# Kernel optimization log

Hardware: AMD Instinct MI355X
Metric: run time of the kernel (lower is better)

Reference implementation:

```python
import jax, jax.numpy as jnp
import numpy as np
import math

def setup_inputs() -> dict:
    key = jax.random.key(0)
    k1, k2, k3 = jax.random.split(key, 3)
    B, S, E = 2, 2048, 1024
    H, D = 16, 64
    inputs = jax.random.normal(k1, (B, S, E), dtype=jnp.float32)
    Wqkv = jax.random.uniform(k2, (E, 3 * H * D), minval=-0.1, maxval=0.1, dtype=jnp.float32)
    Wo = jax.random.uniform(k3, (H * D, E), minval=-0.1, maxval=0.1, dtype=jnp.float32)
    return {"inputs": inputs, "Wqkv": Wqkv, "Wo": Wo, "nhead": H}

def reference(inputs, Wqkv, Wo, nhead):
    B, S, E = inputs.shape
    H = int(nhead)
    D = Wqkv.shape[1] // (3 * H)
    causal, ghost = True, True

    qkv = jnp.matmul(inputs, Wqkv)                       # (B, S, 3*H*D)
    qkv = qkv.reshape(B, S, 3, H, D)
    Q = qkv[:, :, 0].transpose(0, 2, 1, 3)               # (B, H, S, D)
    K = qkv[:, :, 1].transpose(0, 2, 1, 3)
    V = qkv[:, :, 2].transpose(0, 2, 1, 3)

    scores = jnp.einsum('bhqd,bhkd->bhqk', Q, K) / math.sqrt(D)
    if causal:
        neg_inf = jnp.float32(-jnp.inf)
        mask = jnp.where(jnp.triu(jnp.ones((S, S), dtype=bool), k=1), neg_inf, jnp.float32(0.0))
        scores = scores + mask  # broadcast over (B, H)

    # ghost softmax: standard stable softmax but denominator gets +1
    z = jnp.exp(scores - jnp.max(scores, axis=-1, keepdims=True))
    denom = jnp.sum(z, axis=-1, keepdims=True)
    if ghost:
        denom = denom + jnp.float32(1.0)
    attn = z / denom                                      # (B, H, S, S)

    A = jnp.einsum('bhqk,bhkd->bhqd', attn, V)            # (B, H, S, D)
    A = A.transpose(0, 2, 1, 3).reshape(B, S, H * D)      # (B, S, H*D)
    return jnp.matmul(A, Wo)
```

## Files before the change

### kernel.cpp

```cpp
#include <hip/hip_runtime.h>

typedef float    f32x4  __attribute__((ext_vector_type(4)));
typedef _Float16 half8  __attribute__((ext_vector_type(8)));
typedef _Float16 half4v __attribute__((ext_vector_type(4)));

#define MFMA16(a,b,c) __builtin_amdgcn_mfma_f32_16x16x32_f16(a,b,c,0,0,0)

__device__ __forceinline__ float exp2_fast(float x){
  float y; asm("v_exp_f32 %0, %1" : "=v"(y) : "v"(x)); return y;
}
__device__ __forceinline__ void gload_lds16(const _Float16* g, _Float16* l){
  __builtin_amdgcn_global_load_lds(
      (const __attribute__((address_space(1))) unsigned int*)(g),
      (__attribute__((address_space(3))) unsigned int*)(l),
      16, 0, 0);
}

#define S_LEN 2048
#define E_DIM 1024
#define H_NUM 16
#define D_DIM 64
#define NBH   32
#define M_ROWS 4096
#define N3    3072
#define LOG2E 1.44269504089f

__global__ void cast_x_kernel(const float* __restrict__ in,
                              _Float16* __restrict__ hi, int n4){
  int i = blockIdx.x * 256 + threadIdx.x;
  if (i >= n4) return;
  const float4 v = reinterpret_cast<const float4*>(in)[i];
  half4v h;
  h[0] = (_Float16)v.x; h[1] = (_Float16)v.y;
  h[2] = (_Float16)v.z; h[3] = (_Float16)v.w;
  *reinterpret_cast<half4v*>(&hi[i*4]) = h;
}

__global__ void transpose_half(const float* __restrict__ in,
                               _Float16* __restrict__ hi, int R, int C){
  __shared__ float tile[32][33];
  int bx = blockIdx.x * 32, by = blockIdx.y * 32;
  int tx = threadIdx.x & 31, ty = threadIdx.x >> 5;
#pragma unroll
  for (int i = ty; i < 32; i += 8)
    tile[i][tx] = in[(size_t)(by + i) * C + bx + tx];
  __syncthreads();
#pragma unroll
  for (int i = ty; i < 32; i += 8)
    hi[(size_t)(bx + i) * R + by + tx] = (_Float16)tile[tx][i];
}

template<int EPI>
__global__ __launch_bounds__(256, 3) void gemm97(
    const _Float16* __restrict__ A, const _Float16* __restrict__ B,
    int Kdim, int Ndim, float* __restrict__ Cout,
    _Float16* __restrict__ qh, _Float16* __restrict__ kh, _Float16* __restrict__ vh)
{
  __shared__ __align__(16) _Float16 sA[128][64], sB[128][64];
  const int tid = threadIdx.x;
  const int m0 = blockIdx.y * 128, n0 = blockIdx.x * 128;
  const int wid = tid >> 6, lane = tid & 63;
  const int wr = (wid >> 1) * 64, wc = (wid & 1) * 64;
  const int lr = lane & 15, lc = lane >> 4;
  const int ldrow = lane >> 3;
  const int ldcol = ((lane & 7) ^ ldrow) * 8;
  const int swz = (lr & 7) << 4;

  f32x4 acc[4][4] = {};
  const int nK = Kdim >> 6;
  for (int ks = 0; ks < nK; ++ks){
    const int k0 = ks << 6;
#pragma unroll
    for (int cc = 0; cc < 4; ++cc){
      const int c = wid * 4 + cc;
      const int row = c * 8 + ldrow;
      gload_lds16(&A[(size_t)(m0 + row) * Kdim + k0 + ldcol], &sA[c*8][0]);
      gload_lds16(&B[(size_t)(n0 + row) * Kdim + k0 + ldcol], &sB[c*8][0]);
    }
    __syncthreads();
    const char* ab = (const char*)&sA[0][0];
    const char* bb = (const char*)&sB[0][0];
#pragma unroll
    for (int kk = 0; kk < 64; kk += 32){
      half8 fa[4], fb[4];
#pragma unroll
      for (int t = 0; t < 4; ++t){
        fa[t] = *reinterpret_cast<const half8*>(
            ab + (wr + t*16 + lr)*128 + ((kk*2 + lc*16) ^ swz));
        fb[t] = *reinterpret_cast<const half8*>(
            bb + (wc + t*16 + lr)*128 + ((kk*2 + lc*16) ^ swz));
      }
#pragma unroll
      for (int mt = 0; mt < 4; ++mt)
#pragma unroll
        for (int nt = 0; nt < 4; ++nt)
          acc[mt][nt] = MFMA16(fa[mt], fb[nt], acc[mt][nt]);
    }
    __syncthreads();
  }
#pragma unroll
  for (int mt = 0; mt < 4; ++mt)
#pragma unroll
    for (int nt = 0; nt < 4; ++nt)
#pragma unroll
      for (int r = 0; r < 4; ++r){
        const int m = m0 + wr + mt*16 + lc*4 + r;
        const int n = n0 + wc + nt*16 + lr;
        float v = acc[mt][nt][r];
        if (EPI == 0){
          Cout[(size_t)m * Ndim + n] = v;
        } else {
          const int t = n >> 10, rem = n & 1023, hh = rem >> 6, d = rem & 63;
          const int b = m >> 11, s = m & 2047;
          const int bh = b * H_NUM + hh;
          if (t == 0) v *= (0.125f * LOG2E);
          size_t o;
          if (t == 2)  o = ((size_t)bh * D_DIM + d) * S_LEN + s;
          else         o = ((size_t)bh * S_LEN + s) * D_DIM + d;
          _Float16* ph = (t == 0) ? qh : (t == 1) ? kh : vh;
          ph[o] = (_Float16)v;
        }
      }
}

__global__ __launch_bounds__(256, 4) void attn_kernel(
    const _Float16* __restrict__ Qh, const _Float16* __restrict__ Kh,
    const _Float16* __restrict__ Vth, _Float16* __restrict__ Ao)
{
  __shared__ __align__(16) _Float16 sK[2][64][64], sV[2][64][64];
  __shared__ __align__(16) _Float16 sP[4][16][64];
  const int tid = threadIdx.x, wid = tid >> 6, lane = tid & 63;
  const int id  = blockIdx.x + 32 * blockIdx.y;
  const int xcd = id & 7, seq = id >> 3;
  const int bh  = xcd + 8 * (seq & 3);
  const int g = seq >> 2, hsel = g & 7, bsel = g >> 3;
  const int qt = (bsel == 0) ? 31 - hsel
               : (bsel == 1) ? hsel
               : (bsel == 2) ? 23 - hsel
                             : 8 + hsel;
  const int q0 = qt * 64;
  const int nT = qt + 1;
  const int lr = lane & 15, lc = lane >> 4;
  const int swz = (lr & 7) << 4;
  const size_t base = (size_t)bh * S_LEN * D_DIM;

  const int lrow = lane >> 3;
  const int cswz = ((lane & 7) ^ lrow) * 8;

  auto stage = [&](int t, int b){
    const int kv0 = t * 64;
#pragma unroll
    for (int cc = 0; cc < 2; ++cc){
      const int c = wid * 2 + cc;
      const int row = c * 8 + lrow;
      gload_lds16(&Kh[base + (size_t)(kv0 + row) * D_DIM + cswz], &sK[b][c*8][0]);
      gload_lds16(&Vth[base + (size_t)row * S_LEN + kv0 + cswz], &sV[b][c*8][0]);
    }
  };

  const int b = bh >> 4, hh = bh & 15;

  half8 fq[2];
  {
    const int qrow = q0 + wid*16 + lr;
#pragma unroll
    for (int kc = 0; kc < 2; ++kc)
      fq[kc] = *reinterpret_cast<const half8*>(&Qh[base + (size_t)qrow * 64 + kc*32 + lc*8]);
  }

  f32x4 acc[4] = {};
  float m = -1e30f, l = 0.f, tm = -1e30f;

  stage(0, 0);
  __syncthreads();

  int cur = 0;
  for (int t = 0; t < nT; ++t){
    if (t + 1 < nT) stage(t + 1, cur ^ 1);

    const char* kb = (const char*)&sK[cur][0][0];
    f32x4 sc[4];
    __builtin_amdgcn_s_setprio(1);
#pragma unroll
    for (int nt = 0; nt < 4; ++nt){
      f32x4 z = {};
#pragma unroll
      for (int kc = 0; kc < 2; ++kc){
        const half8 fk = *reinterpret_cast<const half8*>(
            kb + (nt*16 + lr)*128 + ((kc*64 + lc*16) ^ swz));
        z = MFMA16(fk, fq[kc], z);
      }
      sc[nt] = z;
    }
    __builtin_amdgcn_s_setprio(0);

    if (t == qt){
#pragma unroll
      for (int nt = 0; nt < 4; ++nt)
#pragma unroll
        for (int r = 0; r < 4; ++r)
          if (nt*16 + lc*4 + r > wid*16 + lr) sc[nt][r] = -1e30f;
    }

    f32x4 a;
#pragma unroll
    for (int j = 0; j < 4; ++j)
      a[j] = fmaxf(fmaxf(sc[0][j], sc[1][j]), fmaxf(sc[2][j], sc[3][j]));
    float mx = fmaxf(fmaxf(a[0], a[1]), fmaxf(a[2], a[3]));
    mx = fmaxf(mx, __shfl_xor(mx, 16));
    mx = fmaxf(mx, __shfl_xor(mx, 32));
    tm = fmaxf(tm, mx);

    if (__any(mx > m + 8.0f)){
      const float mn = fmaxf(m, mx);
      const float s = exp2_fast(m - mn);
      l *= s; m = mn;
      float rs[4];
#pragma unroll
      for (int r = 0; r < 4; ++r)
        rs[r] = __shfl(s, (lc << 4) | (lc*4 + r), 64);
#pragma unroll
      for (int dt = 0; dt < 4; ++dt)
#pragma unroll
        for (int r = 0; r < 4; ++r) acc[dt][r] *= rs[r];
    }

    f32x4 ssum = {};
#pragma unroll
    for (int nt = 0; nt < 4; ++nt){
#pragma unroll
      for (int r = 0; r < 4; ++r) sc[nt][r] = exp2_fast(sc[nt][r] - m);
      ssum += sc[nt];
    }
    float s1 = (ssum[0] + ssum[1]) + (ssum[2] + ssum[3]);
    s1 += __shfl_xor(s1, 16);
    s1 += __shfl_xor(s1, 32);
    l += s1;

    char* pw = (char*)&sP[wid][0][0];
#pragma unroll
    for (int nt = 0; nt < 4; ++nt){
      int2 pk;
      pk.x = __builtin_bit_cast(int, __builtin_amdgcn_cvt_pkrtz(sc[nt][0], sc[nt][1]));
      pk.y = __builtin_bit_cast(int, __builtin_amdgcn_cvt_pkrtz(sc[nt][2], sc[nt][3]));
      *reinterpret_cast<int2*>(pw + lr*128 + ((nt*32 + lc*8) ^ swz)) = pk;
    }

    const half8 pa0 = *reinterpret_cast<const half8*>(pw + lr*128 + ((lc*16) ^ swz));
    const half8 pa1 = *reinterpret_cast<const half8*>(pw + lr*128 + ((64 + lc*16) ^ swz));
    const char* vb = (const char*)&sV[cur][0][0];
    __builtin_amdgcn_s_setprio(1);
#pragma unroll
    for (int dt = 0; dt < 4; ++dt){
#pragma unroll
      for (int kc = 0; kc < 2; ++kc){
        const half8 fv = *reinterpret_cast<const half8*>(
            vb + (dt*16 + lr)*128 + ((kc*64 + lc*16) ^ swz));
        acc[dt] = MFMA16(kc ? pa1 : pa0, fv, acc[dt]);
      }
    }
    __builtin_amdgcn_s_setprio(0);

    __syncthreads();
    cur ^= 1;
  }

  const float den = l + exp2_fast(tm - m);
  float rden[4];
#pragma unroll
  for (int r = 0; r < 4; ++r)
    rden[r] = __shfl(den, (lc << 4) | (lc*4 + r), 64);
#pragma unroll
  for (int dt = 0; dt < 4; ++dt)
#pragma unroll
    for (int r = 0; r < 4; ++r){
      const float o = acc[dt][r] / rden[r];
      const int q = q0 + wid*16 + lc*4 + r;
      const int d = dt*16 + lr;
      Ao[((size_t)(b*S_LEN + q)) * E_DIM + hh*D_DIM + d] = (_Float16)o;
    }
}

extern "C" void kernel_launch(void* const* d_in, const int* in_sizes, int n_in,
                              void* d_out, int out_size, void* d_ws, size_t ws_size,
                              hipStream_t stream){
  const float* X    = (const float*)d_in[0];
  const float* Wqkv = (const float*)d_in[1];
  const float* Wo   = (const float*)d_in[2];
  float* out = (float*)d_out;

  _Float16* w = (_Float16*)d_ws;
  size_t off = 0;
  auto alloc = [&](size_t n){ _Float16* p = w + off; off += n; return p; };
  const size_t ME   = (size_t)M_ROWS * E_DIM;
  const size_t WQ   = (size_t)N3 * E_DIM;
  const size_t WOsz = (size_t)E_DIM * E_DIM;
  const size_t QK   = (size_t)NBH * S_LEN * D_DIM;
  _Float16 *Xh = alloc(ME);
  _Float16 *Wqh = alloc(WQ);
  _Float16 *Woh = alloc(WOsz);
  _Float16 *Qh = alloc(QK), *Kh = alloc(QK), *Vth = alloc(QK);
  _Float16 *Ahalf = alloc(ME);

  cast_x_kernel<<<(int)(ME/4/256), 256, 0, stream>>>(X, Xh, (int)(ME/4));
  transpose_half<<<dim3(N3/32, E_DIM/32), 256, 0, stream>>>(Wqkv, Wqh, E_DIM, N3);
  transpose_half<<<dim3(E_DIM/32, E_DIM/32), 256, 0, stream>>>(Wo, Woh, E_DIM, E_DIM);

  gemm97<1><<<dim3(N3/128, M_ROWS/128), 256, 0, stream>>>(
      Xh, Wqh, E_DIM, N3, nullptr, Qh, Kh, Vth);

  attn_kernel<<<dim3(32, NBH), 256, 0, stream>>>(Qh, Kh, Vth, Ahalf);

  gemm97<0><<<dim3(E_DIM/128, M_ROWS/128), 256, 0, stream>>>(
      Ahalf, Woh, E_DIM, E_DIM, out, nullptr, nullptr, nullptr);
}
```

Before: 124.3 us.

## Single-buffer V in attention and use 64-row tiles for output projection GEMM

Attention now double-buffers only K and keeps a single V buffer. V for the current tile is loaded at the start of each iteration and waited on with an explicit vmcnt plus barrier before the PV MFMAs, which cuts LDS use per block and may allow more resident blocks. The output projection switches to a new 64x128-tile GEMM kernel, doubling the grid from 256 to 512 blocks to fill more CUs. The risks are that V load latency is only partly hidden behind the QK and softmax work, and the new GEMM has no double buffering.

```diff
diff --git a/kernel.cpp b/kernel.cpp
--- a/kernel.cpp
+++ b/kernel.cpp
@@ -123,11 +123,76 @@
       }
 }
 
+__global__ __launch_bounds__(256, 4) void gemm64(
+    const _Float16* __restrict__ A, const _Float16* __restrict__ B,
+    int Kdim, int Ndim, float* __restrict__ Cout)
+{
+  __shared__ __align__(16) _Float16 sA[64][64], sB[128][64];
+  const int tid = threadIdx.x;
+  const int m0 = blockIdx.y * 64, n0 = blockIdx.x * 128;
+  const int wid = tid >> 6, lane = tid & 63;
+  const int wr = (wid >> 1) * 32, wc = (wid & 1) * 64;
+  const int lr = lane & 15, lc = lane >> 4;
+  const int ldrow = lane >> 3;
+  const int ldcol = ((lane & 7) ^ ldrow) * 8;
+  const int swz = (lr & 7) << 4;
+
+  f32x4 acc[2][4] = {};
+  const int nK = Kdim >> 6;
+  for (int ks = 0; ks < nK; ++ks){
+    const int k0 = ks << 6;
+#pragma unroll
+    for (int cc = 0; cc < 2; ++cc){
+      const int c = wid * 2 + cc;
+      const int row = c * 8 + ldrow;
+      gload_lds16(&A[(size_t)(m0 + row) * Kdim + k0 + ldcol], &sA[c*8][0]);
+    }
+#pragma unroll
+    for (int cc = 0; cc < 4; ++cc){
+      const int c = wid * 4 + cc;
+      const int row = c * 8 + ldrow;
+      gload_lds16(&B[(size_t)(n0 + row) * Kdim + k0 + ldcol], &sB[c*8][0]);
+    }
+    __syncthreads();
+    const char* ab = (const char*)&sA[0][0];
+    const char* bb = (const char*)&sB[0][0];
+#pragma unroll
+    for (int kk = 0; kk < 64; kk += 32){
+      half8 fa[2], fb[4];
+#pragma unroll
+      for (int t = 0; t < 2; ++t)
+        fa[t] = *reinterpret_cast<const half8*>(
+            ab + (wr + t*16 + lr)*128 + ((kk*2 + lc*16) ^ swz));
+#pragma unroll
+      for (int t = 0; t < 4; ++t)
+        fb[t] = *reinterpret_cast<const half8*>(
+            bb + (wc + t*16 + lr)*128 + ((kk*2 + lc*16) ^ swz));
+#pragma unroll
+      for (int mt = 0; mt < 2; ++mt)
+#pragma unroll
+        for (int nt = 0; nt < 4; ++nt)
+          acc[mt][nt] = MFMA16(fa[mt], fb[nt], acc[mt][nt]);
+    }
+    __syncthreads();
+  }
+#pragma unroll
+  for (int mt = 0; mt < 2; ++mt)
+#pragma unroll
+    for (int nt = 0; nt < 4; ++nt)
+#pragma unroll
+      for (int r = 0; r < 4; ++r){
+        const int m = m0 + wr + mt*16 + lc*4 + r;
+        const int n = n0 + wc + nt*16 + lr;
+        Cout[(size_t)m * Ndim + n] = acc[mt][nt][r];
+      }
+}
+
 __global__ __launch_bounds__(256, 4) void attn_kernel(
     const _Float16* __restrict__ Qh, const _Float16* __restrict__ Kh,
     const _Float16* __restrict__ Vth, _Float16* __restrict__ Ao)
 {
-  __shared__ __align__(16) _Float16 sK[2][64][64], sV[2][64][64];
+  __shared__ __align__(16) _Float16 sK[2][64][64];
+  __shared__ __align__(16) _Float16 sV[64][64];
   __shared__ __align__(16) _Float16 sP[4][16][64];
   const int tid = threadIdx.x, wid = tid >> 6, lane = tid & 63;
   const int id  = blockIdx.x + 32 * blockIdx.y;
@@ -147,14 +212,22 @@
   const int lrow = lane >> 3;
   const int cswz = ((lane & 7) ^ lrow) * 8;
 
-  auto stage = [&](int t, int b){
+  auto stageK = [&](int t, int b){
     const int kv0 = t * 64;
 #pragma unroll
     for (int cc = 0; cc < 2; ++cc){
       const int c = wid * 2 + cc;
       const int row = c * 8 + lrow;
       gload_lds16(&Kh[base + (size_t)(kv0 + row) * D_DIM + cswz], &sK[b][c*8][0]);
-      gload_lds16(&Vth[base + (size_t)row * S_LEN + kv0 + cswz], &sV[b][c*8][0]);
+    }
+  };
+  auto stageV = [&](int t){
+    const int kv0 = t * 64;
+#pragma unroll
+    for (int cc = 0; cc < 2; ++cc){
+      const int c = wid * 2 + cc;
+      const int row = c * 8 + lrow;
+      gload_lds16(&Vth[base + (size_t)row * S_LEN + kv0 + cswz], &sV[c*8][0]);
     }
   };
 
@@ -171,12 +244,13 @@
   f32x4 acc[4] = {};
   float m = -1e30f, l = 0.f, tm = -1e30f;
 
-  stage(0, 0);
+  stageK(0, 0);
   __syncthreads();
 
   int cur = 0;
   for (int t = 0; t < nT; ++t){
-    if (t + 1 < nT) stage(t + 1, cur ^ 1);
+    stageV(t);
+    if (t + 1 < nT) stageK(t + 1, cur ^ 1);
 
     const char* kb = (const char*)&sK[cur][0][0];
     f32x4 sc[4];
@@ -248,7 +322,13 @@
 
     const half8 pa0 = *reinterpret_cast<const half8*>(pw + lr*128 + ((lc*16) ^ swz));
     const half8 pa1 = *reinterpret_cast<const half8*>(pw + lr*128 + ((64 + lc*16) ^ swz));
-    const char* vb = (const char*)&sV[cur][0][0];
+
+    if (t + 1 < nT) asm volatile("s_waitcnt vmcnt(2)" ::: "memory");
+    else            asm volatile("s_waitcnt vmcnt(0)" ::: "memory");
+    __builtin_amdgcn_sched_barrier(0);
+    __builtin_amdgcn_s_barrier();
+
+    const char* vb = (const char*)&sV[0][0];
     __builtin_amdgcn_s_setprio(1);
 #pragma unroll
     for (int dt = 0; dt < 4; ++dt){
@@ -311,6 +391,6 @@
 
   attn_kernel<<<dim3(32, NBH), 256, 0, stream>>>(Qh, Kh, Vth, Ahalf);
 
-  gemm97<0><<<dim3(E_DIM/128, M_ROWS/128), 256, 0, stream>>>(
-      Ahalf, Woh, E_DIM, E_DIM, out, nullptr, nullptr, nullptr);
-}
+  gemm64<<<dim3(E_DIM/128, M_ROWS/64), 256, 0, stream>>>(
+      Ahalf, Woh, E_DIM, E_DIM, out);
+}
```

Result: faster. 119.4 us (-3.9%).
